# Kernel optimization log

Measured on AMD Instinct MI355X. Metric: run time of the kernel, lower is better.

The kernel has to match this reference:

```python
import jax, jax.numpy as jnp
import numpy as np

B, T, H, L = 32, 256, 1024, 2
FORGET_BIAS = 1.0


def setup_inputs() -> dict:
    key = jax.random.key(0)
    k1, k2, k3, k4 = jax.random.split(key, 4)
    x = jax.random.normal(k1, (B, T, H), dtype=jnp.float32)
    lengths = jax.random.randint(k2, (B,), 1, T + 1, dtype=jnp.int32)
    Wx = jax.random.normal(k3, (L, H, 4 * H), dtype=jnp.float32) * 0.02
    Wh = jax.random.normal(k4, (L, H, 4 * H), dtype=jnp.float32) * 0.02
    b = jnp.zeros((L, 4 * H), dtype=jnp.float32)
    return {"x": x, "lengths": lengths, "Wx": Wx, "Wh": Wh, "b": b}


def _lstm_layer(x, lengths, Wx, Wh, b):
    """One TF-style LSTM layer over time with dynamic_rnn length masking.
    Gate order (i, j, f, o), forget_bias added to f. Returns (outputs, (h_T, c_T))."""
    Bb, Tt, _ = x.shape
    Hh = Wh.shape[0]
    # precompute input projections for all steps: [B, T, 4H]
    xproj = jnp.einsum('bti,ig->btg', x, Wx) + b

    def step(carry, inp):
        h, c = carry
        xt, t = inp  # xt: [B, 4H], t: scalar step index
        z = xt + h @ Wh  # [B, 4H]
        i, j, f, o = jnp.split(z, 4, axis=-1)
        c_new = jax.nn.sigmoid(f + FORGET_BIAS) * c + jax.nn.sigmoid(i) * jnp.tanh(j)
        h_new = jax.nn.sigmoid(o) * jnp.tanh(c_new)
        mask = (t < lengths)[:, None]  # [B,1]
        h2 = jnp.where(mask, h_new, h)
        c2 = jnp.where(mask, c_new, c)
        out = jnp.where(mask, h_new, 0.0)  # dynamic_rnn zeros outputs past length
        return (h2, c2), out

    init = (jnp.zeros((Bb, Hh), x.dtype), jnp.zeros((Bb, Hh), x.dtype))
    (hT, cT), outs = jax.lax.scan(step, init, (xproj.transpose(1, 0, 2), jnp.arange(Tt)))
    return outs.transpose(1, 0, 2), (hT, cT)


def reference(x, lengths, Wx, Wh, b):
    inp = x
    hs, cs = [], []
    for l in range(L):  # fixed small layer stack
        inp, (hT, cT) = _lstm_layer(inp, lengths, Wx[l], Wh[l], b[l])
        hs.append(hT)
        cs.append(cT)
    # rnnout: [B,T,H]; hidden: per-layer final (c,h) like TF LSTMStateTuple
    return inp, jnp.stack(cs), jnp.stack(hs)
```

## Files before the change

### kernel.cpp

```cpp
#include <hip/hip_runtime.h>

typedef unsigned short u16;
typedef unsigned int u32;
typedef unsigned long long u64;
typedef __attribute__((ext_vector_type(8))) short short8;
typedef __attribute__((ext_vector_type(4))) float f32x4;
typedef __attribute__((ext_vector_type(4))) u32 u32x4;
typedef __attribute__((ext_vector_type(2))) u32 u32x2;

#define RN_ 8388608
#define MFMA16(a, b, c) __builtin_amdgcn_mfma_f32_16x16x32_bf16(a, b, c, 0, 0, 0)

__device__ __forceinline__ u16 f2bf(float f) {
  union { float f; u32 u; } v; v.f = f;
  u32 r = v.u + 0x7fffu + ((v.u >> 16) & 1u);
  return (u16)(r >> 16);
}
__device__ __forceinline__ float bf2f(u16 h) {
  union { u32 u; float f; } v; v.u = ((u32)h) << 16;
  return v.f;
}
__device__ __forceinline__ u32 pk2(float a, float b) {
  return (u32)f2bf(a) | ((u32)f2bf(b) << 16);
}
__device__ __forceinline__ int permcol(int R) {
  return (R & 3) * 1024 + ((R >> 5) << 3) + ((R >> 2) & 7);
}
__device__ __forceinline__ float sigm(float x) { return 1.f / (1.f + __expf(-x)); }
__device__ __forceinline__ float tanh_(float x) {
  float e = __expf(2.f * x);
  return 1.f - 2.f / (e + 1.f);
}

__global__ __launch_bounds__(256) void transpose_convert(
    const float* __restrict__ Wx, const float* __restrict__ Wh,
    u16* __restrict__ WxT1, u16* __restrict__ WxT2,
    u16* __restrict__ WhT1, u16* __restrict__ WhT2) {
  __shared__ float lds[64][65];
  const int bid = blockIdx.x, tid = threadIdx.x;
  const int sel = bid >> 10;
  const int tile = bid & 1023;
  const int kt = tile & 15, rt = tile >> 4;
  const float* src;
  u16* dst;
  if (sel == 0)      { src = Wx;                       dst = WxT1; }
  else if (sel == 1) { src = Wx + (size_t)1024 * 4096; dst = WxT2; }
  else if (sel == 2) { src = Wh;                       dst = WhT1; }
  else               { src = Wh + (size_t)1024 * 4096; dst = WhT2; }
#pragma unroll
  for (int ii = 0; ii < 16; ++ii) {
    int idx = ii * 256 + tid;
    int r = idx >> 6, c = idx & 63;
    int run = c >> 3, u = c & 7;
    int blkLoc = run >> 2, gate = run & 3;
    int g = gate * 1024 + (rt * 2 + blkLoc) * 8 + u;
    lds[r][blkLoc * 32 + u * 4 + gate] = src[(size_t)(kt * 64 + r) * 4096 + g];
  }
  __syncthreads();
#pragma unroll
  for (int ii = 0; ii < 16; ++ii) {
    int idx = ii * 256 + tid;
    int rw = idx >> 6, cw = idx & 63;
    dst[(size_t)(rt * 64 + rw) * 1024 + kt * 64 + cw] = f2bf(lds[cw][rw]);
  }
}

template <int IS2>
__device__ void gemm_grp(char* smem, int gb,
    const float* __restrict__ Af32, const u16* __restrict__ Ahp,
    const u16* __restrict__ Bt, const float* __restrict__ bias,
    u16* __restrict__ Cring, const int* flags, int* gdone) {
  u16* As = (u16*)smem;
  u16* Bs = (u16*)(smem + 16384);
  const int tid = threadIdx.x;
  const int lane = tid & 63, w = tid >> 6;
  const int wm = w >> 1, wn = w & 1;
  const int l15 = lane & 15, lq = lane >> 4;
  const int srow = tid >> 2, qd = tid & 3;
  const int mg = gb >> 5, ng = gb & 31;
  const u32 rsw = (u32)((l15 & 7) << 4);

  for (int c = 0; c < 32; ++c) {
    if (w == 0) {
      const int thrA = IS2 ? 8 * (c + 1) : 8 * c - 24;
      const int thrB = 8 * c - 24;
      while (1) {
        bool ok = true;
        if (lane < 16) {
          u32x4 fv;
          const u32x4* fp = (const u32x4*)flags + lane;
          asm volatile("global_load_dwordx4 %0, %1, off sc0 sc1"
                       : "=v"(fv) : "v"(fp) : "memory");
          asm volatile("s_waitcnt vmcnt(0)" ::: "memory");
          __builtin_amdgcn_sched_barrier(0);
          ok = (int)fv[0] >= thrA && (int)fv[1] >= thrA &&
               (int)fv[2] >= thrA && (int)fv[3] >= thrA;
        } else if (IS2 && lane < 32) {
          u32x4 fv;
          const u32x4* fp = (const u32x4*)(flags + 64) + (lane - 16);
          asm volatile("global_load_dwordx4 %0, %1, off sc0 sc1"
                       : "=v"(fv) : "v"(fp) : "memory");
          asm volatile("s_waitcnt vmcnt(0)" ::: "memory");
          __builtin_amdgcn_sched_barrier(0);
          ok = (int)fv[0] >= thrB && (int)fv[1] >= thrB &&
               (int)fv[2] >= thrB && (int)fv[3] >= thrB;
        }
        if (__all(ok)) break;
        __builtin_amdgcn_s_sleep(8);
      }
    }
    __syncthreads();

    f32x4 acc[4][4];
#pragma unroll
    for (int i = 0; i < 4; ++i)
#pragma unroll
      for (int j = 0; j < 4; ++j) acc[i][j] = (f32x4){0.f, 0.f, 0.f, 0.f};

    for (int kt = 0; kt < 16; ++kt) {
      u32x4 aw[2][2], bv[2][2];
#pragma unroll
      for (int rr = 0; rr < 2; ++rr) {
        int row = rr * 64 + srow;
        const u32x4* bp = (const u32x4*)(Bt + (size_t)(ng * 128 + row) * 1024 + kt * 64 + qd * 16);
        bv[rr][0] = bp[0]; bv[rr][1] = bp[1];
        int rg = 256 * c + mg * 128 + row;
        if (IS2) {
          int tq = rg >> 5, b2 = rg & 31;
          int p = kt * 8 + qd * 2;
          const char* ap = (const char*)Ahp + (size_t)tq * 65536 +
                           (size_t)(p * 32 + b2) * 16;
          asm volatile("global_load_dwordx4 %0, %1, off sc0 sc1"
                       : "=v"(aw[rr][0]) : "v"(ap) : "memory");
          asm volatile("global_load_dwordx4 %0, %1, off sc0 sc1"
                       : "=v"(aw[rr][1]) : "v"(ap + 512) : "memory");
        } else {
          const f32x4* ap = (const f32x4*)(Af32 +
              ((size_t)(rg & 31) * 256 + (rg >> 5)) * 1024 + kt * 64 + qd * 16);
          f32x4 a0 = ap[0], a1 = ap[1], a2 = ap[2], a3 = ap[3];
          aw[rr][0][0] = pk2(a0[0], a0[1]); aw[rr][0][1] = pk2(a0[2], a0[3]);
          aw[rr][0][2] = pk2(a1[0], a1[1]); aw[rr][0][3] = pk2(a1[2], a1[3]);
          aw[rr][1][0] = pk2(a2[0], a2[1]); aw[rr][1][1] = pk2(a2[2], a2[3]);
          aw[rr][1][2] = pk2(a3[0], a3[1]); aw[rr][1][3] = pk2(a3[2], a3[3]);
        }
      }
      __syncthreads();
      if (IS2) {
        asm volatile("s_waitcnt vmcnt(0)" ::: "memory");
        __builtin_amdgcn_sched_barrier(0);
      }
#pragma unroll
      for (int rr = 0; rr < 2; ++rr) {
        int row = rr * 64 + srow;
        u32 sw = (u32)((row & 7) << 4);
        int base = row * 128 + qd * 32;
        *(u32x4*)((char*)As + ((base) ^ sw)) = aw[rr][0];
        *(u32x4*)((char*)As + ((base + 16) ^ sw)) = aw[rr][1];
        *(u32x4*)((char*)Bs + ((base) ^ sw)) = bv[rr][0];
        *(u32x4*)((char*)Bs + ((base + 16) ^ sw)) = bv[rr][1];
      }
      __syncthreads();
#pragma unroll
      for (int k2 = 0; k2 < 2; ++k2) {
        short8 af[4], bf[4];
#pragma unroll
        for (int f = 0; f < 4; ++f) {
          af[f] = *(const short8*)((const char*)As +
                   (((wm * 64 + f * 16 + l15) * 128 + k2 * 64 + lq * 16) ^ rsw));
          bf[f] = *(const short8*)((const char*)Bs +
                   (((wn * 64 + f * 16 + l15) * 128 + k2 * 64 + lq * 16) ^ rsw));
        }
#pragma unroll
        for (int fi = 0; fi < 4; ++fi)
#pragma unroll
          for (int fj = 0; fj < 4; ++fj)
            acc[fi][fj] = MFMA16(af[fi], bf[fj], acc[fi][fj]);
      }
    }
#pragma unroll
    for (int fj = 0; fj < 4; ++fj) {
      int gc = ng * 128 + wn * 64 + fj * 16 + l15;
      float bvv = bias[permcol(gc)];
#pragma unroll
      for (int fi = 0; fi < 4; ++fi) {
        int rr0 = (c & 3) * 256 + mg * 128 + wm * 64 + fi * 16 + lq * 4;
#pragma unroll
        for (int r = 0; r < 4; ++r) {
          u32 vv = (u32)f2bf(acc[fi][fj][r] + bvv);
          const u16* cp = Cring + (size_t)(rr0 + r) * 4096 + gc;
          asm volatile("global_store_short %0, %1, off sc0 sc1"
                       :: "v"(cp), "v"(vv) : "memory");
        }
      }
    }
    asm volatile("s_waitcnt vmcnt(0)" ::: "memory");
    __syncthreads();
    if (tid == 0)
      __hip_atomic_fetch_add(gdone + c, 1, __ATOMIC_RELAXED, __HIP_MEMORY_SCOPE_AGENT);
  }
}

#define ISSUE_FRAG(B, i_) do { \
  const int g_ = (i_) >> 2, j_ = (i_) & 3; \
  if (j_ == 0) asm volatile("global_load_dwordx4 %0, %1, off sc0 sc1" \
                            : "=v"(B[i_]) : "v"(pa[g_]) : "memory"); \
  else if (j_ == 1) asm volatile("global_load_dwordx4 %0, %1, off offset:256 sc0 sc1" \
                                 : "=v"(B[i_]) : "v"(pa[g_]) : "memory"); \
  else if (j_ == 2) asm volatile("global_load_dwordx4 %0, %1, off offset:2048 sc0 sc1" \
                                 : "=v"(B[i_]) : "v"(pa[g_]) : "memory"); \
  else asm volatile("global_load_dwordx4 %0, %1, off offset:2304 sc0 sc1" \
                    : "=v"(B[i_]) : "v"(pa[g_]) : "memory"); \
} while (0)
#define DRAIN0() do { asm volatile("s_waitcnt vmcnt(0)" ::: "memory"); \
  __builtin_amdgcn_sched_barrier(0); } while (0)
#define MFALL(B) do { _Pragma("unroll") for (int i_ = 0; i_ < 16; ++i_) { \
  const int ks_ = i_ >> 1, bc_ = i_ & 1; \
  acc[0][bc_] = MFMA16(afr[0][ks_], B[i_], acc[0][bc_]); \
  acc[1][bc_] = MFMA16(afr[1][ks_], B[i_], acc[1][bc_]); \
  acc[2][bc_] = MFMA16(afr[2][ks_], B[i_], acc[2][bc_]); \
  acc[3][bc_] = MFMA16(afr[3][ks_], B[i_], acc[3][bc_]); } } while (0)

template <int L>
__device__ void scan_grp(char* smem, int nb,
    const u16* __restrict__ xpring, const u16* __restrict__ Wt,
    const int* __restrict__ lengths, u64* hpub,
    int* flags_self, const int* gdone,
    float* __restrict__ outp, float* __restrict__ csf, float* __restrict__ hsf) {
  f32x4* partv = (f32x4*)smem;
  u16* h_stage = (u16*)(smem + 32768);
  float* out_stage = (float*)(smem + 33792);
  const int tid = threadIdx.x;
  const int lane = tid & 63, w = tid >> 6;
  const int l15 = lane & 15, q = lane >> 4;
  const int b = (w & 1) * 16 + l15;
  const int u0 = (w >> 1) * 4 + q;
  const int len = lengths[b];

  short8 afr[4][8];
#pragma unroll
  for (int tt = 0; tt < 4; ++tt)
#pragma unroll
    for (int ks = 0; ks < 8; ++ks)
      afr[tt][ks] = *(const short8*)(Wt + (size_t)(nb * 64 + tt * 16 + l15) * 1024 +
                                     w * 256 + ks * 32 + q * 8);

  f32x4 acc[4][2];
#pragma unroll
  for (int tt = 0; tt < 4; ++tt)
#pragma unroll
    for (int bc = 0; bc < 2; ++bc) acc[tt][bc] = (f32x4){0.f, 0.f, 0.f, 0.f};
  float c0 = 0.f, h0 = 0.f, c1 = 0.f, h1 = 0.f;

  const int lane_base = (w * 32 + q) * 512 + l15 * 16;

  for (int t = 0; t < 256; ++t) {
    if ((t & 7) == 0) {
      if (w == 0) {
        const int cidx = t >> 3;
        while (1) {
          bool ok = true;
          if (lane == 0) {
            u32 cd;
            asm volatile("global_load_dword %0, %1, off sc0 sc1"
                         : "=v"(cd) : "v"(gdone + cidx) : "memory");
            asm volatile("s_waitcnt vmcnt(0)" ::: "memory");
            __builtin_amdgcn_sched_barrier(0);
            ok = (int)cd >= 64;
          }
          if (__all(ok)) break;
          __builtin_amdgcn_s_sleep(2);
        }
      }
      __syncthreads();
    }

    const u16* xa = xpring + ((size_t)((t >> 3) & 3) * 256 + (t & 7) * 32 + b) * 4096 +
                    nb * 64 + u0 * 4;
    u32x2 xpv0, xpv1;
    asm volatile("global_load_dwordx2 %0, %1, off sc0 sc1"
                 : "=v"(xpv0) : "v"(xa) : "memory");
    asm volatile("global_load_dwordx2 %0, %1, off sc0 sc1"
                 : "=v"(xpv1) : "v"(xa + 32) : "memory");

    if (t > 0) {
      const char* hp = (const char*)hpub + (size_t)(t - 1) * 65536 + lane_base;
      const char* pa[4];
#pragma unroll
      for (int g = 0; g < 4; ++g) pa[g] = hp + g * 4096;
      short8 bfv[16];
#pragma unroll
      for (int i = 0; i < 16; ++i) ISSUE_FRAG(bfv, i);
      u32 done = 0;
      while (1) {
        DRAIN0();
        {
#pragma unroll
          for (int i = 0; i < 16; ++i) {
            if (!(done & (1u << i))) {
              u32x4 vv = __builtin_bit_cast(u32x4, bfv[i]);
              bool ok = vv[0] != 0xFFFFFFFFu && vv[1] != 0xFFFFFFFFu &&
                        vv[2] != 0xFFFFFFFFu && vv[3] != 0xFFFFFFFFu;
              if (__all(ok)) done |= (1u << i);
            }
          }
        }
        if (done == 0xFFFFu) break;
#pragma unroll
        for (int i = 0; i < 16; ++i)
          if (!(done & (1u << i))) ISSUE_FRAG(bfv, i);
      }
      __builtin_amdgcn_sched_barrier(0);
      MFALL(bfv);
    } else {
      DRAIN0();
    }

#pragma unroll
    for (int tt = 0; tt < 4; ++tt)
#pragma unroll
      for (int bc = 0; bc < 2; ++bc) {
        partv[(w * 8 + tt * 2 + bc) * 64 + lane] = acc[tt][bc];
        acc[tt][bc] = (f32x4){0.f, 0.f, 0.f, 0.f};
      }
    __syncthreads();
    f32x4 s0 = (f32x4){0.f, 0.f, 0.f, 0.f};
    f32x4 s1 = (f32x4){0.f, 0.f, 0.f, 0.f};
#pragma unroll
    for (int w2 = 0; w2 < 4; ++w2) {
      s0 += partv[(w2 * 8 + w) * 64 + lane];
      s1 += partv[(w2 * 8 + 4 + w) * 64 + lane];
    }

    bool mk = t < len;
    {
      float zi = s0[0] + bf2f((u16)(xpv0[0] & 0xffffu));
      float zj = s0[1] + bf2f((u16)(xpv0[0] >> 16));
      float zf = s0[2] + bf2f((u16)(xpv0[1] & 0xffffu)) + 1.f;
      float zo = s0[3] + bf2f((u16)(xpv0[1] >> 16));
      float cn = sigm(zf) * c0 + sigm(zi) * tanh_(zj);
      float hn = sigm(zo) * tanh_(cn);
      c0 = mk ? cn : c0;
      h0 = mk ? hn : h0;
      float ov = mk ? hn : 0.f;
      h_stage[b * 16 + u0] = f2bf(ov);
      if (L) out_stage[b * 16 + u0] = ov;
    }
    {
      float zi = s1[0] + bf2f((u16)(xpv1[0] & 0xffffu));
      float zj = s1[1] + bf2f((u16)(xpv1[0] >> 16));
      float zf = s1[2] + bf2f((u16)(xpv1[1] & 0xffffu)) + 1.f;
      float zo = s1[3] + bf2f((u16)(xpv1[1] >> 16));
      float cn = sigm(zf) * c1 + sigm(zi) * tanh_(zj);
      float hn = sigm(zo) * tanh_(cn);
      c1 = mk ? cn : c1;
      h1 = mk ? hn : h1;
      float ov = mk ? hn : 0.f;
      h_stage[b * 16 + u0 + 8] = f2bf(ov);
      if (L) out_stage[b * 16 + u0 + 8] = ov;
    }
    __syncthreads();

    if (tid < 64) {
      int p = tid >> 5, bb = tid & 31;
      u32x4 pv = *(const u32x4*)((const char*)h_stage + bb * 32 + p * 16);
      char* hd = (char*)hpub + (size_t)t * 65536 +
                 (size_t)((nb * 2 + p) * 32 + bb) * 16;
      asm volatile("global_store_dwordx4 %0, %1, off sc0 sc1"
                   :: "v"(hd), "v"(pv) : "memory");
    }
    if (((t + 1) & 7) == 0 && w == 0) {
      asm volatile("s_waitcnt vmcnt(0)" ::: "memory");
      if (tid == 0)
        __hip_atomic_store(flags_self + nb, t + 1, __ATOMIC_RELAXED,
                           __HIP_MEMORY_SCOPE_AGENT);
    }
    if (L && tid < 128) {
      int bb = tid >> 2, part = tid & 3;
      f32x4 ov = *(const f32x4*)(out_stage + bb * 16 + part * 4);
      *(f32x4*)(outp + ((size_t)bb * 256 + t) * 1024 + nb * 16 + part * 4) = ov;
    }
  }
  csf[L * 32768 + b * 1024 + nb * 16 + u0] = c0;
  csf[L * 32768 + b * 1024 + nb * 16 + u0 + 8] = c1;
  hsf[L * 32768 + b * 1024 + nb * 16 + u0] = h0;
  hsf[L * 32768 + b * 1024 + nb * 16 + u0 + 8] = h1;
}

__global__ __launch_bounds__(256, 1) void lstm_pipe(
    const float* __restrict__ x, const int* __restrict__ lengths,
    const float* __restrict__ bias,
    const u16* __restrict__ WxT1, const u16* __restrict__ WxT2,
    const u16* __restrict__ WhT1, const u16* __restrict__ WhT2,
    u16* xp1ring, u16* xp2ring,
    u64* hpub1, u64* hpub2, int* flags, float* outp) {
  __shared__ __align__(16) char smem[35840];
  int* g1done = flags + 128;
  int* g2done = flags + 160;
  const int bid = blockIdx.x;
  float* csf = outp + RN_;
  float* hsf = csf + 65536;
  if (bid < 64)
    gemm_grp<0>(smem, bid, x, nullptr, WxT1, bias, xp1ring, flags, g1done);
  else if (bid < 128)
    scan_grp<0>(smem, bid - 64, xp1ring, WhT1, lengths, hpub1, flags, g1done,
                outp, csf, hsf);
  else if (bid < 192)
    gemm_grp<1>(smem, bid - 128, nullptr, (const u16*)hpub1, WxT2, bias + 4096,
                xp2ring, flags, g2done);
  else
    scan_grp<1>(smem, bid - 192, xp2ring, WhT2, lengths, hpub2, flags + 64, g2done,
                outp, csf, hsf);
}

#define WS_WXT1 0u
#define WS_WXT2 (8u << 20)
#define WS_WHT1 (16u << 20)
#define WS_WHT2 (24u << 20)
#define WS_XP1 (32u << 20)
#define WS_XP2 (48u << 20)
#define WS_HPUB1 (64u << 20)
#define WS_HPUB2 (80u << 20)
#define WS_FLAGS (96u << 20)

extern "C" void kernel_launch(void* const* d_in, const int* in_sizes, int n_in,
                              void* d_out, int out_size, void* d_ws, size_t ws_size,
                              hipStream_t stream) {
  const float* x = (const float*)d_in[0];
  const int* lengths = (const int*)d_in[1];
  const float* Wx = (const float*)d_in[2];
  const float* Wh = (const float*)d_in[3];
  const float* bias = (const float*)d_in[4];
  float* outp = (float*)d_out;

  if (ws_size < (size_t)WS_FLAGS + 4096) return;

  char* ws = (char*)d_ws;
  u16* WxT1 = (u16*)(ws + WS_WXT1);
  u16* WxT2 = (u16*)(ws + WS_WXT2);
  u16* WhT1 = (u16*)(ws + WS_WHT1);
  u16* WhT2 = (u16*)(ws + WS_WHT2);
  u16* xp1ring = (u16*)(ws + WS_XP1);
  u16* xp2ring = (u16*)(ws + WS_XP2);
  u64* hpub1 = (u64*)(ws + WS_HPUB1);
  u64* hpub2 = (u64*)(ws + WS_HPUB2);
  int* flags = (int*)(ws + WS_FLAGS);

  hipMemsetAsync(flags, 0, 2048, stream);
  hipMemsetAsync(hpub1, 0xFF, 32u << 20, stream);
  transpose_convert<<<4096, 256, 0, stream>>>(Wx, Wh, WxT1, WxT2, WhT1, WhT2);
  lstm_pipe<<<256, 256, 0, stream>>>(x, lengths, bias, WxT1, WxT2, WhT1, WhT2,
                                     xp1ring, xp2ring, hpub1, hpub2, flags, outp);
}
```

Baseline: 1.255 ms.

## Publish hidden state directly from each lane and defer progress flag update

Each thread now writes its bf16 hidden value straight to the global publish buffer with a short store, removing the LDS staging buffer and the 64-thread vector store. The check for sentinel values (0xFFFF) is now done per 16-bit element, since each half is written separately. The per-8-step progress flag is moved to after the next step's barrier, which already implies the prior stores completed, so the explicit vmcnt wait on the publish path goes away. The trade-off is many small uncoalesced global stores in place of a few wide ones. Correctness also now depends on ordering being implied by the barrier and drain rather than an explicit wait before the flag.

```diff
diff --git a/kernel.cpp b/kernel.cpp
--- a/kernel.cpp
+++ b/kernel.cpp
@@ -227,8 +227,7 @@
     int* flags_self, const int* gdone,
     float* __restrict__ outp, float* __restrict__ csf, float* __restrict__ hsf) {
   f32x4* partv = (f32x4*)smem;
-  u16* h_stage = (u16*)(smem + 32768);
-  float* out_stage = (float*)(smem + 33792);
+  float* out_stage = (float*)(smem + 32768);
   const int tid = threadIdx.x;
   const int lane = tid & 63, w = tid >> 6;
   const int l15 = lane & 15, q = lane >> 4;
@@ -252,6 +251,7 @@
   float c0 = 0.f, h0 = 0.f, c1 = 0.f, h1 = 0.f;
 
   const int lane_base = (w * 32 + q) * 512 + l15 * 16;
+  const int pub_base = nb * 1024 + b * 16 + u0 * 2;
 
   for (int t = 0; t < 256; ++t) {
     if ((t & 7) == 0) {
@@ -298,8 +298,12 @@
           for (int i = 0; i < 16; ++i) {
             if (!(done & (1u << i))) {
               u32x4 vv = __builtin_bit_cast(u32x4, bfv[i]);
-              bool ok = vv[0] != 0xFFFFFFFFu && vv[1] != 0xFFFFFFFFu &&
-                        vv[2] != 0xFFFFFFFFu && vv[3] != 0xFFFFFFFFu;
+              bool ok = true;
+#pragma unroll
+              for (int k = 0; k < 4; ++k) {
+                ok = ok && ((vv[k] & 0xFFFFu) != 0xFFFFu) &&
+                     (vv[k] < 0xFFFF0000u);
+              }
               if (__all(ok)) done |= (1u << i);
             }
           }
@@ -323,6 +327,9 @@
         acc[tt][bc] = (f32x4){0.f, 0.f, 0.f, 0.f};
       }
     __syncthreads();
+    if ((t & 7) == 0 && t > 0 && tid == 0)
+      __hip_atomic_store(flags_self + nb, t, __ATOMIC_RELAXED,
+                         __HIP_MEMORY_SCOPE_AGENT);
     f32x4 s0 = (f32x4){0.f, 0.f, 0.f, 0.f};
     f32x4 s1 = (f32x4){0.f, 0.f, 0.f, 0.f};
 #pragma unroll
@@ -332,6 +339,7 @@
     }
 
     bool mk = t < len;
+    char* hb = (char*)hpub + (size_t)t * 65536 + pub_base;
     {
       float zi = s0[0] + bf2f((u16)(xpv0[0] & 0xffffu));
       float zj = s0[1] + bf2f((u16)(xpv0[0] >> 16));
@@ -342,7 +350,9 @@
       c0 = mk ? cn : c0;
       h0 = mk ? hn : h0;
       float ov = mk ? hn : 0.f;
-      h_stage[b * 16 + u0] = f2bf(ov);
+      u32 pv = (u32)f2bf(ov);
+      asm volatile("global_store_short %0, %1, off sc0 sc1"
+                   :: "v"(hb), "v"(pv) : "memory");
       if (L) out_stage[b * 16 + u0] = ov;
     }
     {
@@ -355,31 +365,24 @@
       c1 = mk ? cn : c1;
       h1 = mk ? hn : h1;
       float ov = mk ? hn : 0.f;
-      h_stage[b * 16 + u0 + 8] = f2bf(ov);
+      u32 pv = (u32)f2bf(ov);
+      asm volatile("global_store_short %0, %1, off sc0 sc1"
+                   :: "v"(hb + 512), "v"(pv) : "memory");
       if (L) out_stage[b * 16 + u0 + 8] = ov;
     }
     __syncthreads();
 
-    if (tid < 64) {
-      int p = tid >> 5, bb = tid & 31;
-      u32x4 pv = *(const u32x4*)((const char*)h_stage + bb * 32 + p * 16);
-      char* hd = (char*)hpub + (size_t)t * 65536 +
-                 (size_t)((nb * 2 + p) * 32 + bb) * 16;
-      asm volatile("global_store_dwordx4 %0, %1, off sc0 sc1"
-                   :: "v"(hd), "v"(pv) : "memory");
-    }
-    if (((t + 1) & 7) == 0 && w == 0) {
-      asm volatile("s_waitcnt vmcnt(0)" ::: "memory");
-      if (tid == 0)
-        __hip_atomic_store(flags_self + nb, t + 1, __ATOMIC_RELAXED,
-                           __HIP_MEMORY_SCOPE_AGENT);
-    }
     if (L && tid < 128) {
       int bb = tid >> 2, part = tid & 3;
       f32x4 ov = *(const f32x4*)(out_stage + bb * 16 + part * 4);
       *(f32x4*)(outp + ((size_t)bb * 256 + t) * 1024 + nb * 16 + part * 4) = ov;
     }
   }
+  DRAIN0();
+  __syncthreads();
+  if (tid == 0)
+    __hip_atomic_store(flags_self + nb, 256, __ATOMIC_RELAXED,
+                       __HIP_MEMORY_SCOPE_AGENT);
   csf[L * 32768 + b * 1024 + nb * 16 + u0] = c0;
   csf[L * 32768 + b * 1024 + nb * 16 + u0 + 8] = c1;
   hsf[L * 32768 + b * 1024 + nb * 16 + u0] = h0;
```

After: 1.354 ms. 1.08x slower.
